# Kernel tuning notes

Hardware: AMD Instinct MI355X
Metric: run time of the kernel (lower is better)

Reference implementation:

```python
import jax, jax.numpy as jnp
import numpy as np

B, T, D, DFF, E = 4, 2048, 1024, 4096, 8


def setup_inputs() -> dict:
    key = jax.random.key(0)
    ks = jax.random.split(key, 4)
    s_in = 1.0 / np.sqrt(D)
    s_ff = 1.0 / np.sqrt(DFF)
    return {
        "x": jax.random.normal(ks[0], (B, T, D), dtype=jnp.float32),
        "gate_W": jax.random.normal(ks[1], (D, E), dtype=jnp.float32) * s_in,
        "gate_b": jnp.zeros((E,), dtype=jnp.float32),
        "W1": jax.random.normal(ks[2], (E, D, DFF), dtype=jnp.float32) * s_in,
        "b1": jnp.zeros((E, DFF), dtype=jnp.float32),
        "W2": jax.random.normal(ks[3], (E, DFF, D), dtype=jnp.float32) * s_ff,
        "b2": jnp.zeros((E, D), dtype=jnp.float32),
    }


def reference(x, gate_W, gate_b, W1, b1, W2, b2):
    # x: [B, T, D]. Top-1 gated MoE; each expert FFN runs on the (masked)
    # full token set, exactly as the original dense-masked implementation.
    b, t, d = x.shape
    num_experts = gate_W.shape[-1]
    logits = jnp.einsum("btd,de->bte", x, gate_W) + gate_b  # [B,T,E]
    top1 = jnp.argmax(logits, axis=-1).reshape(-1)          # [B*T]
    flat_x = x.reshape(b * t, d)                            # [N,D]
    out = jnp.zeros_like(flat_x)
    for e in range(num_experts):  # small fixed expert count
        mask = (top1 == e).astype(x.dtype)[:, None]         # [N,1]
        h = jax.nn.gelu((flat_x * mask) @ W1[e] + b1[e], approximate=False)
        out = out + (h @ W2[e] + b2[e]) * mask
    return out.reshape(b, t, d)
```

## Files before the change

kernel.cpp:

```cpp
#include <hip/hip_runtime.h>
#include <hip/hip_bf16.h>
#include <cstdint>

#define N_TOK 8192
#define D_IN  1024
#define DFF   4096
#define NE    8
#define DEPTH 3

typedef __bf16 bf16x8 __attribute__((ext_vector_type(8)));
typedef float  f32x4  __attribute__((ext_vector_type(4)));

__device__ __forceinline__ unsigned short f2bf(float f) {
  unsigned u = __float_as_uint(f);
  u += 0x7fffu + ((u >> 16) & 1u);
  return (unsigned short)(u >> 16);
}

__device__ __forceinline__ void gll16(const void* g, void* l) {
  __builtin_amdgcn_global_load_lds(
      (__attribute__((address_space(1))) void*)g,
      (__attribute__((address_space(3))) void*)l, 16, 0, 0);
}

__global__ __launch_bounds__(256) void gate_kernel(
    const float* __restrict__ x, const float* __restrict__ gW,
    const float* __restrict__ gb, unsigned short* __restrict__ xbf,
    int* __restrict__ counts, int* __restrict__ perm) {
  int wave = threadIdx.x >> 6, lane = threadIdx.x & 63;
  int n = blockIdx.x * 4 + wave;
  const float* xr = x + (size_t)n * D_IN;
  double acc[NE];
#pragma unroll
  for (int e = 0; e < NE; ++e) acc[e] = 0.0;
#pragma unroll
  for (int j = 0; j < 16; ++j) {
    int d = j * 64 + lane;
    float v = xr[d];
    xbf[(size_t)n * D_IN + d] = f2bf(v);
    float4 g0 = *(const float4*)(gW + (size_t)d * 8);
    float4 g1 = *(const float4*)(gW + (size_t)d * 8 + 4);
    acc[0] += (double)v * (double)g0.x;
    acc[1] += (double)v * (double)g0.y;
    acc[2] += (double)v * (double)g0.z;
    acc[3] += (double)v * (double)g0.w;
    acc[4] += (double)v * (double)g1.x;
    acc[5] += (double)v * (double)g1.y;
    acc[6] += (double)v * (double)g1.z;
    acc[7] += (double)v * (double)g1.w;
  }
#pragma unroll
  for (int m = 32; m >= 1; m >>= 1) {
#pragma unroll
    for (int e = 0; e < NE; ++e) acc[e] += __shfl_xor(acc[e], m);
  }
  if (lane == 0) {
    float best = (float)acc[0] + gb[0];
    int be = 0;
#pragma unroll
    for (int e = 1; e < NE; ++e) {
      float lv = (float)acc[e] + gb[e];
      if (lv > best) { best = lv; be = e; }
    }
    int pos = atomicAdd(&counts[be], 1);
    perm[be * N_TOK + pos] = n;
  }
}

__global__ void plan_kernel(int* __restrict__ hdr, int* __restrict__ tile_e,
                            int* __restrict__ tile_m, int* __restrict__ sub0,
                            int* __restrict__ tile_e2, int* __restrict__ tile_m2) {
  if (threadIdx.x != 0 || blockIdx.x != 0) return;
  int off = 0;
  for (int e = 0; e < NE; ++e) { hdr[8 + e] = off; off += hdr[e]; }
  hdr[16] = off;
  int n1 = 0, n2 = 0;
  for (int e = 0; e < NE; ++e) {
    int Me = hdr[e];
    int base2 = n2;
    for (int m2 = 0; m2 < Me; m2 += 64) { tile_e2[n2] = e; tile_m2[n2] = m2; ++n2; }
    for (int m0 = 0; m0 < Me; m0 += 128) {
      tile_e[n1] = e; tile_m[n1] = m0; sub0[n1] = base2 + (m0 >> 6); ++n1;
    }
  }
  hdr[17] = n1;
  hdr[18] = n2;
}

__global__ __launch_bounds__(256) void apack_kernel(
    const unsigned short* __restrict__ xbf, const int* __restrict__ hdr,
    const int* __restrict__ tile_e, const int* __restrict__ tile_m,
    const int* __restrict__ perm, unsigned short* __restrict__ Apack) {
  int wi = blockIdx.x >> 2;
  if (wi >= hdr[17]) return;
  int q = blockIdx.x & 3;
  int e = tile_e[wi], m0 = tile_m[wi], Me = hdr[e];
  int wave = threadIdx.x >> 6, lane = threadIdx.x & 63;
  int kq = lane >> 4, m = lane & 15;
#pragma unroll
  for (int s = 0; s < 2; ++s) {
    int g = wave * 2 + s;
    int r = m0 + g * 16 + m;
    if (r >= Me) r = Me - 1;
    int token = perm[e * N_TOK + r];
    const char* src = (const char*)xbf + (size_t)token * 2048 + kq * 16;
    char* dst = (char*)Apack + (size_t)wi * 32 * 8192 + g * 1024 + lane * 16;
    for (int kk = q * 8; kk < q * 8 + 8; ++kk)
      *(int4*)(dst + (size_t)kk * 8192) = *(const int4*)(src + kk * 64);
  }
}

__global__ __launch_bounds__(256) void wpack_kernel(
    const float* __restrict__ src, unsigned short* __restrict__ dst,
    int R, int C, int tiles_r, int tiles_c) {
  __shared__ unsigned short tile[64][72];
  int tpe = tiles_r * tiles_c;
  int e = blockIdx.x / tpe;
  int t = blockIdx.x % tpe;
  int r0 = (t / tiles_c) * 64, c0 = (t % tiles_c) * 64;
  const float* s = src + (size_t)e * R * C;
  int tr = threadIdx.x >> 4, tc = (threadIdx.x & 15) * 4;
#pragma unroll
  for (int p = 0; p < 4; ++p) {
    int row = r0 + tr + p * 16;
    const float4 v = *(const float4*)(s + (size_t)row * C + c0 + tc);
    tile[tc + 0][tr + p * 16] = f2bf(v.x);
    tile[tc + 1][tr + p * 16] = f2bf(v.y);
    tile[tc + 2][tr + p * 16] = f2bf(v.z);
    tile[tc + 3][tr + p * 16] = f2bf(v.w);
  }
  __syncthreads();
  int nkk = R >> 5, ntc = C >> 7;
#pragma unroll
  for (int u = 0; u < 2; ++u) {
    int c = u * 256 + threadIdx.x;
    int kk_l = c >> 8, gg_l = (c >> 6) & 3, kq = (c >> 4) & 3, mm = c & 15;
    int fl = gg_l * 16 + mm;
    int kl = kk_l * 32 + kq * 8;
    int4 val = *(const int4*)&tile[fl][kl];
    int f = c0 + fl;
    int nt = f >> 7, gg = (f >> 4) & 7;
    int kk = (r0 >> 5) + kk_l;
    size_t off = ((((size_t)e * ntc + nt) * nkk + kk) * 8 + gg) * 1024 + (kq * 16 + mm) * 16;
    *(int4*)((char*)dst + off) = val;
  }
}

__global__ __launch_bounds__(256) void gemm1(
    const unsigned short* __restrict__ Apack, const unsigned short* __restrict__ Bpack1,
    const float* __restrict__ b1, const int* __restrict__ hdr,
    const int* __restrict__ tile_e, const int* __restrict__ tile_m,
    const int* __restrict__ sub0, unsigned short* __restrict__ Hpack) {
  int wi = blockIdx.x >> 5;
  if (wi >= hdr[17]) return;
  int nt = blockIdx.x & 31;
  int e = tile_e[wi];
  int m0 = tile_m[wi];
  int Me = hdr[e];
  int n0 = nt * 128;

  __shared__ __align__(16) char smem[49152];
  char* Asm = smem;
  char* Bsm = smem + 24576;

  int tid = threadIdx.x, wave = tid >> 6, lane = tid & 63;
  int wm = wave >> 1, wn = wave & 1;

  const char* abase = (const char*)Apack + (size_t)wi * 32 * 8192;
  const char* bbase = (const char*)Bpack1 + (size_t)(e * 32 + nt) * 32 * 8192;
  int off0 = (wave * 2 + 0) * 1024 + lane * 16;
  int off1 = (wave * 2 + 1) * 1024 + lane * 16;

  const int NITER = D_IN / 32;
#pragma unroll
  for (int p = 0; p < DEPTH; ++p) {
    gll16(abase + (size_t)p * 8192 + off0, Asm + p * 8192 + off0);
    gll16(abase + (size_t)p * 8192 + off1, Asm + p * 8192 + off1);
    gll16(bbase + (size_t)p * 8192 + off0, Bsm + p * 8192 + off0);
    gll16(bbase + (size_t)p * 8192 + off1, Bsm + p * 8192 + off1);
  }

  f32x4 acc[4][4];
#pragma unroll
  for (int i = 0; i < 4; ++i)
#pragma unroll
    for (int j = 0; j < 4; ++j) { f32x4 z = {0.f, 0.f, 0.f, 0.f}; acc[i][j] = z; }

  int cur = 0;
  for (int kk = 0; kk < NITER; ++kk) {
    asm volatile("s_waitcnt vmcnt(8)" ::: "memory");
    __builtin_amdgcn_s_barrier();
    const char* ab = Asm + cur * 8192;
    const char* bb = Bsm + cur * 8192;
    bf16x8 af[4], bfv[4];
#pragma unroll
    for (int i = 0; i < 4; ++i)
      af[i] = *(const bf16x8*)(ab + (wm * 4 + i) * 1024 + lane * 16);
#pragma unroll
    for (int j = 0; j < 4; ++j)
      bfv[j] = *(const bf16x8*)(bb + (wn * 4 + j) * 1024 + lane * 16);
    asm volatile("s_waitcnt lgkmcnt(0)" ::: "memory");
    __builtin_amdgcn_s_barrier();
    int nx = kk + DEPTH;
    if (nx > NITER - 1) nx = NITER - 1;
    char* ad = Asm + cur * 8192;
    char* bd = Bsm + cur * 8192;
    gll16(abase + (size_t)nx * 8192 + off0, ad + off0);
    gll16(abase + (size_t)nx * 8192 + off1, ad + off1);
    gll16(bbase + (size_t)nx * 8192 + off0, bd + off0);
    gll16(bbase + (size_t)nx * 8192 + off1, bd + off1);
#pragma unroll
    for (int i = 0; i < 4; ++i)
#pragma unroll
      for (int j = 0; j < 4; ++j)
        acc[i][j] = __builtin_amdgcn_mfma_f32_16x16x32_bf16(af[i], bfv[j], acc[i][j], 0, 0, 0);
    cur = (cur == DEPTH - 1) ? 0 : cur + 1;
  }

  asm volatile("s_waitcnt vmcnt(0)" ::: "memory");
  __syncthreads();
  unsigned short* Cl = (unsigned short*)smem;
  int quad = lane >> 4, col_l = lane & 15;
#pragma unroll
  for (int i = 0; i < 4; ++i) {
#pragma unroll
    for (int j = 0; j < 4; ++j) {
      int f = n0 + wn * 64 + j * 16 + col_l;
      float bb = b1[(size_t)e * DFF + f];
      int lc = wn * 64 + j * 16 + col_l;
#pragma unroll
      for (int r = 0; r < 4; ++r) {
        int lr = wm * 64 + i * 16 + quad * 4 + r;
        float v = acc[i][j][r] + bb;
        v = 0.5f * v * (1.0f + erff(v * 0.70710678118654752f));
        Cl[lr * 128 + lc] = f2bf(v);
      }
    }
  }
  __syncthreads();
  int s0 = sub0[wi];
  bool hasB = (m0 + 64 < Me);
#pragma unroll
  for (int u = 0; u < 8; ++u) {
    int c = u * 256 + tid;
    int lr = c >> 4, fc = c & 15;
    int sv = lr >> 6;
    if (sv == 1 && !hasB) continue;
    int4 val = *(const int4*)(Cl + lr * 128 + fc * 8);
    int wi2 = s0 + sv;
    int m2 = lr & 63;
    int gg = m2 >> 4, mm = m2 & 15;
    int kk2 = nt * 4 + (fc >> 2), kq2 = fc & 3;
    *(int4*)((char*)Hpack + ((size_t)wi2 * 128 + kk2) * 4096 + gg * 1024 + (kq2 * 16 + mm) * 16) = val;
  }
}

__global__ __launch_bounds__(256) void gemm2(
    const unsigned short* __restrict__ Hpack, const unsigned short* __restrict__ Bpack2,
    const float* __restrict__ b2, const int* __restrict__ hdr,
    const int* __restrict__ tile_e2, const int* __restrict__ tile_m2,
    const int* __restrict__ perm, float* __restrict__ out) {
  int wi = blockIdx.x >> 3;
  if (wi >= hdr[18]) return;
  int nt = blockIdx.x & 7;
  int e = tile_e2[wi];
  int m0 = tile_m2[wi];
  int Me = hdr[e];
  int n0 = nt * 128;

  __shared__ __align__(16) char smem[36864];
  char* Asm = smem;
  char* Bsm = smem + 12288;

  int tid = threadIdx.x, wave = tid >> 6, lane = tid & 63;
  int wm2 = wave >> 1, wn = wave & 1;

  const char* abase = (const char*)Hpack + (size_t)wi * 128 * 4096;
  const char* bbase = (const char*)Bpack2 + (size_t)(e * 8 + nt) * 128 * 8192;
  int aoff = wave * 1024 + lane * 16;
  int off0 = (wave * 2 + 0) * 1024 + lane * 16;
  int off1 = (wave * 2 + 1) * 1024 + lane * 16;

  const int NITER = DFF / 32;
#pragma unroll
  for (int p = 0; p < DEPTH; ++p) {
    gll16(abase + (size_t)p * 4096 + aoff, Asm + p * 4096 + aoff);
    gll16(bbase + (size_t)p * 8192 + off0, Bsm + p * 8192 + off0);
    gll16(bbase + (size_t)p * 8192 + off1, Bsm + p * 8192 + off1);
  }

  f32x4 acc[2][4];
#pragma unroll
  for (int i = 0; i < 2; ++i)
#pragma unroll
    for (int j = 0; j < 4; ++j) { f32x4 z = {0.f, 0.f, 0.f, 0.f}; acc[i][j] = z; }

  int cur = 0;
  for (int kk = 0; kk < NITER; ++kk) {
    asm volatile("s_waitcnt vmcnt(6)" ::: "memory");
    __builtin_amdgcn_s_barrier();
    const char* ab = Asm + cur * 4096;
    const char* bb = Bsm + cur * 8192;
    bf16x8 af[2], bfv[4];
#pragma unroll
    for (int i = 0; i < 2; ++i)
      af[i] = *(const bf16x8*)(ab + (wm2 * 2 + i) * 1024 + lane * 16);
#pragma unroll
    for (int j = 0; j < 4; ++j)
      bfv[j] = *(const bf16x8*)(bb + (wn * 4 + j) * 1024 + lane * 16);
    asm volatile("s_waitcnt lgkmcnt(0)" ::: "memory");
    __builtin_amdgcn_s_barrier();
    int nx = kk + DEPTH;
    if (nx > NITER - 1) nx = NITER - 1;
    char* ad = Asm + cur * 4096;
    char* bd = Bsm + cur * 8192;
    gll16(abase + (size_t)nx * 4096 + aoff, ad + aoff);
    gll16(bbase + (size_t)nx * 8192 + off0, bd + off0);
    gll16(bbase + (size_t)nx * 8192 + off1, bd + off1);
#pragma unroll
    for (int i = 0; i < 2; ++i)
#pragma unroll
      for (int j = 0; j < 4; ++j)
        acc[i][j] = __builtin_amdgcn_mfma_f32_16x16x32_bf16(af[i], bfv[j], acc[i][j], 0, 0, 0);
    cur = (cur == DEPTH - 1) ? 0 : cur + 1;
  }

  int quad = lane >> 4, col_l = lane & 15;
#pragma unroll
  for (int i = 0; i < 2; ++i) {
    int rbase = m0 + wm2 * 32 + i * 16 + quad * 4;
#pragma unroll
    for (int j = 0; j < 4; ++j) {
      int col = n0 + wn * 64 + j * 16 + col_l;
      float bb = b2[(size_t)e * D_IN + col];
#pragma unroll
      for (int r = 0; r < 4; ++r) {
        int rr = rbase + r;
        if (rr < Me) {
          int token = perm[e * N_TOK + rr];
          out[(size_t)token * D_IN + col] = acc[i][j][r] + bb;
        }
      }
    }
  }
}

extern "C" void kernel_launch(void* const* d_in, const int* in_sizes, int n_in,
                              void* d_out, int out_size, void* d_ws, size_t ws_size,
                              hipStream_t stream) {
  const float* x  = (const float*)d_in[0];
  const float* gW = (const float*)d_in[1];
  const float* gb = (const float*)d_in[2];
  const float* W1 = (const float*)d_in[3];
  const float* b1 = (const float*)d_in[4];
  const float* W2 = (const float*)d_in[5];
  const float* b2 = (const float*)d_in[6];
  float* out = (float*)d_out;

  char* ws = (char*)d_ws;
  int* hdr     = (int*)ws;
  int* tile_e  = (int*)(ws + 4096);
  int* tile_m  = (int*)(ws + 4608);
  int* sub0    = (int*)(ws + 5120);
  int* tile_e2 = (int*)(ws + 5632);
  int* tile_m2 = (int*)(ws + 6656);
  int* perm    = (int*)(ws + 16384);
  unsigned short* xbf    = (unsigned short*)(ws + 524288);
  unsigned short* Bpack2 = (unsigned short*)(ws + 524288);
  unsigned short* Apack  = (unsigned short*)(ws + 69206016);
  unsigned short* Bpack1 = (unsigned short*)(ws + 92274688);
  unsigned short* Hpack  = (unsigned short*)(ws + 159383552);

  hipMemsetAsync(hdr, 0, 256, stream);
  gate_kernel<<<N_TOK / 4, 256, 0, stream>>>(x, gW, gb, xbf, hdr, perm);
  plan_kernel<<<1, 64, 0, stream>>>(hdr, tile_e, tile_m, sub0, tile_e2, tile_m2);
  apack_kernel<<<71 * 4, 256, 0, stream>>>(xbf, hdr, tile_e, tile_m, perm, Apack);
  wpack_kernel<<<NE * 16 * 64, 256, 0, stream>>>(W1, Bpack1, D_IN, DFF, 16, 64);
  wpack_kernel<<<NE * 64 * 16, 256, 0, stream>>>(W2, Bpack2, DFF, D_IN, 64, 16);
  gemm1<<<71 * 32, 256, 0, stream>>>(Apack, Bpack1, b1, hdr, tile_e, tile_m, sub0, Hpack);
  gemm2<<<135 * 8, 256, 0, stream>>>(Hpack, Bpack2, b2, hdr, tile_e2, tile_m2, perm, out);
}
```

Measured before the change: 651.7 us.

## Enlarge gemm2 tile to 128 rows, merge weight packing, replace atomics routing

Routing now writes top1 per token and a single 1024-thread build kernel computes counts, offsets, tile plans and the permutation with shared-memory atomics. This removes the memset, the global atomics and the serial plan kernel. The two weight-packing launches are merged into one kernel. gemm2 now uses 128-row M tiles built from two 64-row Hpack sub-tiles, which doubles B reuse and halves the number of gemm2 blocks. The cost is more registers and LDS per block and fewer blocks in flight.

```diff
diff --git a/kernel.cpp b/kernel.cpp
--- a/kernel.cpp
+++ b/kernel.cpp
@@ -26,7 +26,7 @@
 __global__ __launch_bounds__(256) void gate_kernel(
     const float* __restrict__ x, const float* __restrict__ gW,
     const float* __restrict__ gb, unsigned short* __restrict__ xbf,
-    int* __restrict__ counts, int* __restrict__ perm) {
+    int* __restrict__ top1) {
   int wave = threadIdx.x >> 6, lane = threadIdx.x & 63;
   int n = blockIdx.x * 4 + wave;
   const float* xr = x + (size_t)n * D_IN;
@@ -62,29 +62,53 @@
       float lv = (float)acc[e] + gb[e];
       if (lv > best) { best = lv; be = e; }
     }
-    int pos = atomicAdd(&counts[be], 1);
-    perm[be * N_TOK + pos] = n;
-  }
-}
-
-__global__ void plan_kernel(int* __restrict__ hdr, int* __restrict__ tile_e,
-                            int* __restrict__ tile_m, int* __restrict__ sub0,
-                            int* __restrict__ tile_e2, int* __restrict__ tile_m2) {
-  if (threadIdx.x != 0 || blockIdx.x != 0) return;
-  int off = 0;
-  for (int e = 0; e < NE; ++e) { hdr[8 + e] = off; off += hdr[e]; }
-  hdr[16] = off;
-  int n1 = 0, n2 = 0;
-  for (int e = 0; e < NE; ++e) {
-    int Me = hdr[e];
-    int base2 = n2;
-    for (int m2 = 0; m2 < Me; m2 += 64) { tile_e2[n2] = e; tile_m2[n2] = m2; ++n2; }
-    for (int m0 = 0; m0 < Me; m0 += 128) {
-      tile_e[n1] = e; tile_m[n1] = m0; sub0[n1] = base2 + (m0 >> 6); ++n1;
+    top1[n] = be;
+  }
+}
+
+__global__ __launch_bounds__(1024) void build_kernel(
+    const int* __restrict__ top1, int* __restrict__ hdr, int* __restrict__ perm,
+    int* __restrict__ tile_e, int* __restrict__ tile_m, int* __restrict__ sub0) {
+  __shared__ int cnt[NE];
+  int tid = threadIdx.x;
+  if (tid < NE) cnt[tid] = 0;
+  __syncthreads();
+  int mye[8], myp[8];
+#pragma unroll
+  for (int r = 0; r < 8; ++r) {
+    int n = r * 1024 + tid;
+    int e = top1[n];
+    mye[r] = e;
+    myp[r] = atomicAdd(&cnt[e], 1);
+  }
+  __syncthreads();
+  if (tid == 0) {
+    int o = 0;
+    int n1 = 0, n2 = 0;
+    for (int e = 0; e < NE; ++e) {
+      int Me = cnt[e];
+      hdr[e] = Me;
+      hdr[8 + e] = o;
+      o += Me;
     }
-  }
-  hdr[17] = n1;
-  hdr[18] = n2;
+    hdr[16] = o;
+    for (int e = 0; e < NE; ++e) {
+      int Me = cnt[e];
+      int base2 = n2;
+      n2 += (Me + 63) >> 6;
+      for (int m0 = 0; m0 < Me; m0 += 128) {
+        tile_e[n1] = e; tile_m[n1] = m0; sub0[n1] = base2 + (m0 >> 6); ++n1;
+      }
+    }
+    hdr[17] = n1;
+    hdr[18] = n2;
+  }
+  __syncthreads();
+#pragma unroll
+  for (int r = 0; r < 8; ++r) {
+    int n = r * 1024 + tid;
+    perm[mye[r] * N_TOK + myp[r]] = n;
+  }
 }
 
 __global__ __launch_bounds__(256) void apack_kernel(
@@ -105,18 +129,18 @@
     int token = perm[e * N_TOK + r];
     const char* src = (const char*)xbf + (size_t)token * 2048 + kq * 16;
     char* dst = (char*)Apack + (size_t)wi * 32 * 8192 + g * 1024 + lane * 16;
-    for (int kk = q * 8; kk < q * 8 + 8; ++kk)
-      *(int4*)(dst + (size_t)kk * 8192) = *(const int4*)(src + kk * 64);
-  }
-}
-
-__global__ __launch_bounds__(256) void wpack_kernel(
+    for (int kk = 0; kk < 8; ++kk)
+      *(int4*)(dst + (size_t)(q * 8 + kk) * 8192) = *(const int4*)(src + (q * 8 + kk) * 64);
+  }
+}
+
+__device__ __forceinline__ void wpack_body(
     const float* __restrict__ src, unsigned short* __restrict__ dst,
-    int R, int C, int tiles_r, int tiles_c) {
+    int R, int C, int tiles_r, int tiles_c, int bid) {
   __shared__ unsigned short tile[64][72];
   int tpe = tiles_r * tiles_c;
-  int e = blockIdx.x / tpe;
-  int t = blockIdx.x % tpe;
+  int e = bid / tpe;
+  int t = bid % tpe;
   int r0 = (t / tiles_c) * 64, c0 = (t % tiles_c) * 64;
   const float* s = src + (size_t)e * R * C;
   int tr = threadIdx.x >> 4, tc = (threadIdx.x & 15) * 4;
@@ -144,6 +168,15 @@
     size_t off = ((((size_t)e * ntc + nt) * nkk + kk) * 8 + gg) * 1024 + (kq * 16 + mm) * 16;
     *(int4*)((char*)dst + off) = val;
   }
+}
+
+__global__ __launch_bounds__(256) void wpack_both(
+    const float* __restrict__ W1, unsigned short* __restrict__ B1,
+    const float* __restrict__ W2, unsigned short* __restrict__ B2) {
+  if (blockIdx.x < NE * 16 * 64)
+    wpack_body(W1, B1, D_IN, DFF, 16, 64, blockIdx.x);
+  else
+    wpack_body(W2, B2, DFF, D_IN, 64, 16, blockIdx.x - NE * 16 * 64);
 }
 
 __global__ __launch_bounds__(256) void gemm1(
@@ -258,53 +291,64 @@
 __global__ __launch_bounds__(256) void gemm2(
     const unsigned short* __restrict__ Hpack, const unsigned short* __restrict__ Bpack2,
     const float* __restrict__ b2, const int* __restrict__ hdr,
-    const int* __restrict__ tile_e2, const int* __restrict__ tile_m2,
-    const int* __restrict__ perm, float* __restrict__ out) {
+    const int* __restrict__ tile_e, const int* __restrict__ tile_m,
+    const int* __restrict__ sub0, const int* __restrict__ perm,
+    float* __restrict__ out) {
   int wi = blockIdx.x >> 3;
-  if (wi >= hdr[18]) return;
+  if (wi >= hdr[17]) return;
   int nt = blockIdx.x & 7;
-  int e = tile_e2[wi];
-  int m0 = tile_m2[wi];
+  int e = tile_e[wi];
+  int m0 = tile_m[wi];
   int Me = hdr[e];
   int n0 = nt * 128;
-
-  __shared__ __align__(16) char smem[36864];
+  int s0 = sub0[wi];
+  int s1 = (m0 + 64 < Me) ? s0 + 1 : s0;
+
+  __shared__ __align__(16) char smem[49152];
   char* Asm = smem;
-  char* Bsm = smem + 12288;
+  char* Bsm = smem + 24576;
 
   int tid = threadIdx.x, wave = tid >> 6, lane = tid & 63;
-  int wm2 = wave >> 1, wn = wave & 1;
-
-  const char* abase = (const char*)Hpack + (size_t)wi * 128 * 4096;
+  int wm = wave >> 1, wn = wave & 1;
+
+  const char* abase_s[2];
+  int agl[2];
+  int off_s[2];
+#pragma unroll
+  for (int s = 0; s < 2; ++s) {
+    int g = wave * 2 + s;
+    int sv = g >> 2;
+    abase_s[s] = (const char*)Hpack + (size_t)((sv ? s1 : s0) * 128) * 4096;
+    agl[s] = (g & 3) * 1024 + lane * 16;
+    off_s[s] = g * 1024 + lane * 16;
+  }
   const char* bbase = (const char*)Bpack2 + (size_t)(e * 8 + nt) * 128 * 8192;
-  int aoff = wave * 1024 + lane * 16;
-  int off0 = (wave * 2 + 0) * 1024 + lane * 16;
-  int off1 = (wave * 2 + 1) * 1024 + lane * 16;
 
   const int NITER = DFF / 32;
 #pragma unroll
   for (int p = 0; p < DEPTH; ++p) {
-    gll16(abase + (size_t)p * 4096 + aoff, Asm + p * 4096 + aoff);
-    gll16(bbase + (size_t)p * 8192 + off0, Bsm + p * 8192 + off0);
-    gll16(bbase + (size_t)p * 8192 + off1, Bsm + p * 8192 + off1);
-  }
-
-  f32x4 acc[2][4];
-#pragma unroll
-  for (int i = 0; i < 2; ++i)
+    gll16(abase_s[0] + (size_t)p * 4096 + agl[0], Asm + p * 8192 + off_s[0]);
+    gll16(abase_s[1] + (size_t)p * 4096 + agl[1], Asm + p * 8192 + off_s[1]);
+    gll16(bbase + (size_t)p * 8192 + off_s[0], Bsm + p * 8192 + off_s[0]);
+    gll16(bbase + (size_t)p * 8192 + off_s[1], Bsm + p * 8192 + off_s[1]);
+  }
+
+  f32x4 acc[4][4];
+#pragma unroll
+  for (int i = 0; i < 4; ++i)
 #pragma unroll
     for (int j = 0; j < 4; ++j) { f32x4 z = {0.f, 0.f, 0.f, 0.f}; acc[i][j] = z; }
 
   int cur = 0;
   for (int kk = 0; kk < NITER; ++kk) {
-    asm volatile("s_waitcnt vmcnt(6)" ::: "memory");
+    asm volatile("s_waitcnt vmcnt(8)" ::: "memory");
     __builtin_amdgcn_s_barrier();
-    const char* ab = Asm + cur * 4096;
+    const char* ab = Asm + cur * 8192;
     const char* bb = Bsm + cur * 8192;
-    bf16x8 af[2], bfv[4];
-#pragma unroll
-    for (int i = 0; i < 2; ++i)
-      af[i] = *(const bf16x8*)(ab + (wm2 * 2 + i) * 1024 + lane * 16);
+    bf16x8 af[4], bfv[4];
+#pragma unroll
+    for (int i = 0; i < 4; ++i)
+      af[i] = *(const bf16x8*)(ab + (wm * 4 + i) * 1024 + lane * 16);
 #pragma unroll
     for (int j = 0; j < 4; ++j)
       bfv[j] = *(const bf16x8*)(bb + (wn * 4 + j) * 1024 + lane * 16);
@@ -312,13 +356,14 @@
     __builtin_amdgcn_s_barrier();
     int nx = kk + DEPTH;
     if (nx > NITER - 1) nx = NITER - 1;
-    char* ad = Asm + cur * 4096;
+    char* ad = Asm + cur * 8192;
     char* bd = Bsm + cur * 8192;
-    gll16(abase + (size_t)nx * 4096 + aoff, ad + aoff);
-    gll16(bbase + (size_t)nx * 8192 + off0, bd + off0);
-    gll16(bbase + (size_t)nx * 8192 + off1, bd + off1);
-#pragma unroll
-    for (int i = 0; i < 2; ++i)
+    gll16(abase_s[0] + (size_t)nx * 4096 + agl[0], ad + off_s[0]);
+    gll16(abase_s[1] + (size_t)nx * 4096 + agl[1], ad + off_s[1]);
+    gll16(bbase + (size_t)nx * 8192 + off_s[0], bd + off_s[0]);
+    gll16(bbase + (size_t)nx * 8192 + off_s[1], bd + off_s[1]);
+#pragma unroll
+    for (int i = 0; i < 4; ++i)
 #pragma unroll
       for (int j = 0; j < 4; ++j)
         acc[i][j] = __builtin_amdgcn_mfma_f32_16x16x32_bf16(af[i], bfv[j], acc[i][j], 0, 0, 0);
@@ -327,8 +372,8 @@
 
   int quad = lane >> 4, col_l = lane & 15;
 #pragma unroll
-  for (int i = 0; i < 2; ++i) {
-    int rbase = m0 + wm2 * 32 + i * 16 + quad * 4;
+  for (int i = 0; i < 4; ++i) {
+    int rbase = m0 + wm * 64 + i * 16 + quad * 4;
 #pragma unroll
     for (int j = 0; j < 4; ++j) {
       int col = n0 + wn * 64 + j * 16 + col_l;
@@ -362,21 +407,18 @@
   int* tile_e  = (int*)(ws + 4096);
   int* tile_m  = (int*)(ws + 4608);
   int* sub0    = (int*)(ws + 5120);
-  int* tile_e2 = (int*)(ws + 5632);
-  int* tile_m2 = (int*)(ws + 6656);
-  int* perm    = (int*)(ws + 16384);
+  int* top1    = (int*)(ws + 8192);
+  int* perm    = (int*)(ws + 65536);
   unsigned short* xbf    = (unsigned short*)(ws + 524288);
   unsigned short* Bpack2 = (unsigned short*)(ws + 524288);
   unsigned short* Apack  = (unsigned short*)(ws + 69206016);
   unsigned short* Bpack1 = (unsigned short*)(ws + 92274688);
   unsigned short* Hpack  = (unsigned short*)(ws + 159383552);
 
-  hipMemsetAsync(hdr, 0, 256, stream);
-  gate_kernel<<<N_TOK / 4, 256, 0, stream>>>(x, gW, gb, xbf, hdr, perm);
-  plan_kernel<<<1, 64, 0, stream>>>(hdr, tile_e, tile_m, sub0, tile_e2, tile_m2);
+  gate_kernel<<<N_TOK / 4, 256, 0, stream>>>(x, gW, gb, xbf, top1);
+  build_kernel<<<1, 1024, 0, stream>>>(top1, hdr, perm, tile_e, tile_m, sub0);
   apack_kernel<<<71 * 4, 256, 0, stream>>>(xbf, hdr, tile_e, tile_m, perm, Apack);
-  wpack_kernel<<<NE * 16 * 64, 256, 0, stream>>>(W1, Bpack1, D_IN, DFF, 16, 64);
-  wpack_kernel<<<NE * 64 * 16, 256, 0, stream>>>(W2, Bpack2, DFF, D_IN, 64, 16);
+  wpack_both<<<NE * 16 * 64 + NE * 64 * 16, 256, 0, stream>>>(W1, Bpack1, W2, Bpack2);
   gemm1<<<71 * 32, 256, 0, stream>>>(Apack, Bpack1, b1, hdr, tile_e, tile_m, sub0, Hpack);
-  gemm2<<<135 * 8, 256, 0, stream>>>(Hpack, Bpack2, b2, hdr, tile_e2, tile_m2, perm, out);
-}
+  gemm2<<<71 * 8, 256, 0, stream>>>(Hpack, Bpack2, b2, hdr, tile_e, tile_m, sub0, perm, out);
+}
```

Result: faster. 570.2 us (-12.5%).
